# Kernel optimization log

Measured on AMD Instinct MI355X. Metric: run time of the kernel, lower is better.

## Reference

```python
import jax, jax.numpy as jnp
import numpy as np

B, S, D, H, DK = 2, 2048, 1024, 16, 64
NEG = -1000000000.0


def setup_inputs() -> dict:
    key = jax.random.key(0)
    ks = jax.random.split(key, 7)
    scale = 1.0 / np.sqrt(D)
    return {
        "pos_encode_toks": jax.random.normal(ks[0], (B, S, D), dtype=jnp.float32),
        "Wq": jax.random.uniform(ks[1], (D, D), minval=-scale, maxval=scale, dtype=jnp.float32),
        "bq": jax.random.uniform(ks[2], (D,), minval=-scale, maxval=scale, dtype=jnp.float32),
        "Wk": jax.random.uniform(ks[3], (D, D), minval=-scale, maxval=scale, dtype=jnp.float32),
        "bk": jax.random.uniform(ks[4], (D,), minval=-scale, maxval=scale, dtype=jnp.float32),
        "W0": jax.random.uniform(ks[5], (D, D), minval=-scale, maxval=scale, dtype=jnp.float32),
        "b0": jax.random.uniform(ks[6], (D,), minval=-scale, maxval=scale, dtype=jnp.float32),
    }


def reference(pos_encode_toks, Wq, bq, Wk, bk, W0, b0):
    x = pos_encode_toks
    b, s, d = x.shape
    # NOTE: the original module computes V with Wq (a bug in the source) -- replicated here.
    q = (x @ Wq + bq).reshape(b, s, H, DK).transpose(0, 2, 1, 3)  # [B,H,S,DK]
    k = (x @ Wk + bk).reshape(b, s, H, DK).transpose(0, 2, 1, 3)
    v = q  # V = Wq(x), same projection as Q
    scores = jnp.einsum("bhqd,bhkd->bhqk", q, k) / np.sqrt(DK)
    causal = jnp.tril(jnp.ones((s, s), dtype=bool))
    scores = jnp.where(causal, scores, NEG)
    att_pat = jax.nn.softmax(scores, axis=-1)
    att = jnp.einsum("bhqk,bhkd->bhqd", att_pat, v)
    att = att.transpose(0, 2, 1, 3).reshape(b, s, d)
    return att @ W0 + b0
```

## Files before the change

kernel.cpp:

```cpp
#include <hip/hip_runtime.h>
#include <hip/hip_bf16.h>
#include <cstdint>
#include <cstddef>


#define AS1 __attribute__((address_space(1)))
#define AS3 __attribute__((address_space(3)))

typedef unsigned short u16;
typedef __attribute__((ext_vector_type(8))) short bf16x8;
typedef __attribute__((ext_vector_type(4))) float f32x4;

__device__ __forceinline__ u16 f2bf(float f) {
  uint32_t u = __builtin_bit_cast(uint32_t, f);
  u += 0x7fffu + ((u >> 16) & 1u);
  return (u16)(u >> 16);
}

__device__ __forceinline__ void gload16(const void* g, void* l) {
  __builtin_amdgcn_global_load_lds((const AS1 uint32_t*)(uintptr_t)g,
                                   (AS3 uint32_t*)(uintptr_t)l, 16, 0, 0);
}

__global__ __launch_bounds__(256) void cvt_x_kernel(const float* __restrict__ x,
                                                    u16* __restrict__ xb) {
  const int stride = gridDim.x * blockDim.x;
  int i = blockIdx.x * blockDim.x + threadIdx.x;
  const float4* x4 = (const float4*)x;
  ushort4* o4 = (ushort4*)xb;
  for (; i < 1048576; i += stride) {
    float4 v = x4[i];
    ushort4 o;
    o.x = f2bf(v.x); o.y = f2bf(v.y); o.z = f2bf(v.z); o.w = f2bf(v.w);
    o4[i] = o;
  }
}

__global__ __launch_bounds__(256) void transpose_w_kernel(
    const float* __restrict__ Wq, const float* __restrict__ Wk,
    const float* __restrict__ W0, u16* __restrict__ wqT,
    u16* __restrict__ wkT, u16* __restrict__ w0T) {
  const float* src; u16* dst;
  if (blockIdx.z == 0)      { src = Wq; dst = wqT; }
  else if (blockIdx.z == 1) { src = Wk; dst = wkT; }
  else                      { src = W0; dst = w0T; }
  __shared__ u16 T[64][65];
  const int k0 = blockIdx.y * 64, n0 = blockIdx.x * 64;
  const int c = threadIdx.x & 63, r0 = threadIdx.x >> 6;
#pragma unroll
  for (int i = 0; i < 16; ++i) {
    int r = i * 4 + r0;
    T[r][c] = f2bf(src[(size_t)(k0 + r) * 1024 + n0 + c]);
  }
  __syncthreads();
#pragma unroll
  for (int i = 0; i < 16; ++i) {
    int r = i * 4 + r0;
    dst[(size_t)(n0 + r) * 1024 + k0 + c] = T[c][r];
  }
}

__global__ __launch_bounds__(256) void transpose_q_kernel(const u16* __restrict__ q,
                                                          u16* __restrict__ qT) {
  const int bh = blockIdx.y;
  const int s0 = blockIdx.x * 64;
  const u16* src = q + (size_t)bh * 2048 * 64;
  u16* dst = qT + (size_t)bh * 64 * 2048;
  __shared__ u16 T[64][65];
  const int c = threadIdx.x & 63, r0 = threadIdx.x >> 6;
#pragma unroll
  for (int i = 0; i < 16; ++i) {
    int r = i * 4 + r0;
    T[r][c] = src[(size_t)(s0 + r) * 64 + c];
  }
  __syncthreads();
#pragma unroll
  for (int i = 0; i < 16; ++i) {
    int r = i * 4 + r0;
    dst[(size_t)r * 2048 + s0 + c] = T[c][r];
  }
}

template <int EPI, int NTILES>
__global__ __launch_bounds__(512, 4) void gemm_kernel(
    const u16* __restrict__ A, const u16* __restrict__ BT,
    const float* __restrict__ bias0, const float* __restrict__ bias1,
    u16* __restrict__ Oq, u16* __restrict__ Ok, float* __restrict__ Of) {
  __shared__ __align__(16) u16 As[128][64];
  __shared__ __align__(16) u16 Bs[128][64];
  const int tid = threadIdx.x, wid = tid >> 6, lane = tid & 63;
  const int l15 = lane & 15, lg = lane >> 4;
  constexpr int NH = NTILES / 2;
  const int bid = blockIdx.x;
  const int c = bid & 7, l = bid >> 3;
  const int m0 = ((c >> 1) * 8 + l / NH) * 128;
  const int n0 = ((c & 1) * NH + l % NH) * 128;
  const int wrow = (wid >> 2) * 64, wcol = (wid & 3) * 32;
  const int srow = lane >> 3;
  const int gz = ((lane & 7) ^ srow) * 8;

  f32x4 acc[4][2] = {};

  for (int k0 = 0; k0 < 1024; k0 += 64) {
#pragma unroll
    for (int i = 0; i < 2; ++i) {
      int ch = wid * 2 + i;
      gload16(&A[(size_t)(m0 + ch * 8 + srow) * 1024 + k0 + gz], &As[ch * 8][0]);
      gload16(&BT[(size_t)(n0 + ch * 8 + srow) * 1024 + k0 + gz], &Bs[ch * 8][0]);
    }
    __syncthreads();
#pragma unroll
    for (int kf = 0; kf < 2; ++kf) {
      const int cg = ((kf * 4 + lg) ^ (lane & 7)) * 8;
      bf16x8 af[4], bfr[2];
#pragma unroll
      for (int m = 0; m < 4; ++m)
        af[m] = *(const bf16x8*)&As[wrow + m * 16 + l15][cg];
#pragma unroll
      for (int n = 0; n < 2; ++n)
        bfr[n] = *(const bf16x8*)&Bs[wcol + n * 16 + l15][cg];
#pragma unroll
      for (int m = 0; m < 4; ++m)
#pragma unroll
        for (int n = 0; n < 2; ++n)
          acc[m][n] = __builtin_amdgcn_mfma_f32_16x16x32_bf16(af[m], bfr[n], acc[m][n], 0, 0, 0);
    }
    __syncthreads();
  }

  float bv[2];
#pragma unroll
  for (int n = 0; n < 2; ++n) {
    const int gn = n0 + wcol + n * 16 + l15;
    if constexpr (EPI == 0)
      bv[n] = (gn < 1024) ? bias0[gn] : bias1[gn - 1024];
    else
      bv[n] = bias0[gn];
  }
#pragma unroll
  for (int m = 0; m < 4; ++m) {
#pragma unroll
    for (int r = 0; r < 4; ++r) {
      const int gm = m0 + wrow + m * 16 + lg * 4 + r;
#pragma unroll
      for (int n = 0; n < 2; ++n) {
        const int gn = n0 + wcol + n * 16 + l15;
        float v = acc[m][n][r] + bv[n];
        if constexpr (EPI == 2) {
          Of[(size_t)gm * 1024 + gn] = v;
        } else {
          u16* dst = (gn < 1024) ? Oq : Ok;
          const int gg = gn & 1023;
          const int b = gm >> 11, s = gm & 2047;
          const int h = gg >> 6, dk = gg & 63;
          dst[(((size_t)(b * 16 + h)) * 2048 + s) * 64 + dk] = f2bf(v);
        }
      }
    }
  }
}

__global__ __launch_bounds__(256, 4) void attn_kernel(const u16* __restrict__ Q,
                                                      const u16* __restrict__ K,
                                                      const u16* __restrict__ QT,
                                                      u16* __restrict__ ATT) {
  __shared__ __align__(16) u16 Ks[2][64][64];
  __shared__ __align__(16) u16 Vs[2][64][64];
  __shared__ __align__(16) u16 Ps[4][16][64];
  const int tid = threadIdx.x, wid = tid >> 6, lane = tid & 63;
  const int l15 = lane & 15, lg = lane >> 4;
  const int bid = blockIdx.x;
  const int bh = bid & 31;
  const int qt = 31 - (bid >> 5);
  const size_t base = (size_t)bh * 2048 * 64;
  const int bb = bh >> 4, hh = bh & 15;
  const int srow = lane >> 3;
  const int gz = ((lane & 7) ^ srow) * 8;
  const float SCALE2 = 0.18033688011112042f;

  const int q0 = qt * 64;
  const int wrow = q0 + wid * 16;

  bf16x8 qf[2];
#pragma unroll
  for (int kf = 0; kf < 2; ++kf)
    qf[kf] = *(const bf16x8*)&Q[base + (size_t)(wrow + l15) * 64 + kf * 32 + lg * 8];

  f32x4 o[4] = {};
  float mx[4], sm[4];
#pragma unroll
  for (int r = 0; r < 4; ++r) { mx[r] = -3e38f; sm[r] = 0.f; }

#pragma unroll
  for (int i = 0; i < 2; ++i) {
    int ch = wid * 2 + i;
    gload16(&K[base + (size_t)(ch * 8 + srow) * 64 + gz], &Ks[0][ch * 8][0]);
    gload16(&QT[base + (size_t)(ch * 8 + srow) * 2048 + gz], &Vs[0][ch * 8][0]);
  }
  __syncthreads();

  for (int t = 0; t <= qt; ++t) {
    const int cur = t & 1;
    if (t < qt) {
      const int kv1 = (t + 1) * 64;
#pragma unroll
      for (int i = 0; i < 2; ++i) {
        int ch = wid * 2 + i;
        gload16(&K[base + (size_t)(kv1 + ch * 8 + srow) * 64 + gz], &Ks[cur ^ 1][ch * 8][0]);
        gload16(&QT[base + (size_t)(ch * 8 + srow) * 2048 + kv1 + gz], &Vs[cur ^ 1][ch * 8][0]);
      }
    }

    f32x4 sc[4] = {};
#pragma unroll
    for (int kf = 0; kf < 2; ++kf) {
      const int cg = ((kf * 4 + lg) ^ (lane & 7)) * 8;
      bf16x8 kb[4];
#pragma unroll
      for (int n = 0; n < 4; ++n)
        kb[n] = *(const bf16x8*)&Ks[cur][n * 16 + l15][cg];
      __builtin_amdgcn_s_setprio(1);
#pragma unroll
      for (int n = 0; n < 4; ++n)
        sc[n] = __builtin_amdgcn_mfma_f32_16x16x32_bf16(qf[kf], kb[n], sc[n], 0, 0, 0);
      __builtin_amdgcn_s_setprio(0);
    }

    const bool maskt = (t == qt);
    float pr[4][4], rmax[4];
#pragma unroll
    for (int n = 0; n < 4; ++n)
#pragma unroll
      for (int r = 0; r < 4; ++r) {
        float v = sc[n][r] * SCALE2;
        if (maskt && (n * 16 + l15 > wid * 16 + lg * 4 + r)) v = -1e30f;
        pr[n][r] = v;
      }
#pragma unroll
    for (int r = 0; r < 4; ++r) {
      rmax[r] = fmaxf(fmaxf(pr[0][r], pr[1][r]), fmaxf(pr[2][r], pr[3][r]));
#pragma unroll
      for (int d = 1; d < 16; d <<= 1)
        rmax[r] = fmaxf(rmax[r], __shfl_xor(rmax[r], d));
    }

    bool grow = false;
#pragma unroll
    for (int r = 0; r < 4; ++r) grow |= (rmax[r] > mx[r] + 8.0f);
    if (__any(grow)) {
#pragma unroll
      for (int r = 0; r < 4; ++r) {
        const float mnew = fmaxf(mx[r], rmax[r]);
        const float alpha = exp2f(mx[r] - mnew);
        mx[r] = mnew;
        sm[r] *= alpha;
#pragma unroll
        for (int n = 0; n < 4; ++n) o[n][r] *= alpha;
      }
    }
#pragma unroll
    for (int r = 0; r < 4; ++r) {
      float rs = 0.f;
#pragma unroll
      for (int n = 0; n < 4; ++n) {
        const float p = exp2f(pr[n][r] - mx[r]);
        pr[n][r] = p;
        rs += p;
      }
      sm[r] += rs;
    }

#pragma unroll
    for (int r = 0; r < 4; ++r) {
      const int prow = lg * 4 + r;
      const int sw = (prow & 7) << 3;
      __hip_bfloat162 c01 = __float22bfloat162_rn(make_float2(pr[0][r], pr[1][r]));
      __hip_bfloat162 c23 = __float22bfloat162_rn(make_float2(pr[2][r], pr[3][r]));
      u16* pp = &Ps[wid][prow][0];
      pp[(l15)      ^ sw] = __builtin_bit_cast(u16, c01.x);
      pp[(16 + l15) ^ sw] = __builtin_bit_cast(u16, c01.y);
      pp[(32 + l15) ^ sw] = __builtin_bit_cast(u16, c23.x);
      pp[(48 + l15) ^ sw] = __builtin_bit_cast(u16, c23.y);
    }
    asm volatile("s_waitcnt lgkmcnt(0)" ::: "memory");

#pragma unroll
    for (int kf = 0; kf < 2; ++kf) {
      const int cg = ((kf * 4 + lg) ^ (lane & 7)) * 8;
      bf16x8 pa = *(const bf16x8*)&Ps[wid][l15][cg];
      bf16x8 vb[4];
#pragma unroll
      for (int n = 0; n < 4; ++n)
        vb[n] = *(const bf16x8*)&Vs[cur][n * 16 + l15][cg];
      __builtin_amdgcn_s_setprio(1);
#pragma unroll
      for (int n = 0; n < 4; ++n)
        o[n] = __builtin_amdgcn_mfma_f32_16x16x32_bf16(pa, vb[n], o[n], 0, 0, 0);
      __builtin_amdgcn_s_setprio(0);
    }
    __syncthreads();
  }

#pragma unroll
  for (int r = 0; r < 4; ++r)
#pragma unroll
    for (int d = 1; d < 16; d <<= 1) sm[r] += __shfl_xor(sm[r], d);

#pragma unroll
  for (int r = 0; r < 4; ++r) {
    const float inv = 1.0f / sm[r];
    const int s = wrow + lg * 4 + r;
    __hip_bfloat162 c01 = __float22bfloat162_rn(make_float2(o[0][r] * inv, o[1][r] * inv));
    __hip_bfloat162 c23 = __float22bfloat162_rn(make_float2(o[2][r] * inv, o[3][r] * inv));
    u16* dst = &ATT[((size_t)(bb * 2048 + s)) * 1024 + hh * 64 + l15];
    dst[0]  = __builtin_bit_cast(u16, c01.x);
    dst[16] = __builtin_bit_cast(u16, c01.y);
    dst[32] = __builtin_bit_cast(u16, c23.x);
    dst[48] = __builtin_bit_cast(u16, c23.y);
  }
}

extern "C" void kernel_launch(void* const* d_in, const int* in_sizes, int n_in,
                              void* d_out, int out_size, void* d_ws, size_t ws_size,
                              hipStream_t stream) {
  const float* x  = (const float*)d_in[0];
  const float* Wq = (const float*)d_in[1];
  const float* bq = (const float*)d_in[2];
  const float* Wk = (const float*)d_in[3];
  const float* bk = (const float*)d_in[4];
  const float* W0 = (const float*)d_in[5];
  const float* b0 = (const float*)d_in[6];
  float* out = (float*)d_out;

  char* ws = (char*)d_ws;
  u16* xb  = (u16*)(ws + 0);
  u16* wqT = (u16*)(ws + 8388608);
  u16* wkT = (u16*)(ws + 10485760);
  u16* w0T = (u16*)(ws + 12582912);
  u16* q   = (u16*)(ws + 14680064);
  u16* k   = (u16*)(ws + 23068672);
  u16* qT  = (u16*)(ws + 31457280);
  u16* att = (u16*)(ws + 39845888);

  cvt_x_kernel<<<dim3(1024), dim3(256), 0, stream>>>(x, xb);
  transpose_w_kernel<<<dim3(16, 16, 3), dim3(256), 0, stream>>>(Wq, Wk, W0, wqT, wkT, w0T);
  gemm_kernel<0, 16><<<dim3(512), dim3(512), 0, stream>>>(xb, wqT, bq, bk, q, k, nullptr);
  transpose_q_kernel<<<dim3(32, 32), dim3(256), 0, stream>>>(q, qT);
  attn_kernel<<<dim3(1024), dim3(256), 0, stream>>>(q, k, qT, att);
  gemm_kernel<2, 8><<<dim3(256), dim3(512), 0, stream>>>(att, w0T, b0, nullptr, nullptr, nullptr, out);
}
```

Measured before the change: 183.8 us.

## Fuse prep kernels, write Q transpose from GEMM, transpose attention score layout

Merges the x conversion and weight transpose into one launch, and drops the separate Q transpose kernel by having the QK projection GEMM epilogue also write Q transposed. The softmax scale is folded into K at projection time. The attention MFMAs are swapped to compute S^T so each lane owns one query row, which cuts the row reductions to two shuffles and allows packed P and output stores. The price is strided scalar stores for the transposed Q in the GEMM epilogue, plus rounding K to bf16 after scaling.

```diff
diff --git a/kernel.cpp b/kernel.cpp
--- a/kernel.cpp
+++ b/kernel.cpp
@@ -16,36 +16,42 @@
   u += 0x7fffu + ((u >> 16) & 1u);
   return (u16)(u >> 16);
 }
+__device__ __forceinline__ uint32_t pk2bf(float a, float b) {
+  return (uint32_t)f2bf(a) | ((uint32_t)f2bf(b) << 16);
+}
 
 __device__ __forceinline__ void gload16(const void* g, void* l) {
   __builtin_amdgcn_global_load_lds((const AS1 uint32_t*)(uintptr_t)g,
                                    (AS3 uint32_t*)(uintptr_t)l, 16, 0, 0);
 }
 
-__global__ __launch_bounds__(256) void cvt_x_kernel(const float* __restrict__ x,
-                                                    u16* __restrict__ xb) {
-  const int stride = gridDim.x * blockDim.x;
-  int i = blockIdx.x * blockDim.x + threadIdx.x;
-  const float4* x4 = (const float4*)x;
-  ushort4* o4 = (ushort4*)xb;
-  for (; i < 1048576; i += stride) {
-    float4 v = x4[i];
-    ushort4 o;
-    o.x = f2bf(v.x); o.y = f2bf(v.y); o.z = f2bf(v.z); o.w = f2bf(v.w);
-    o4[i] = o;
-  }
-}
-
-__global__ __launch_bounds__(256) void transpose_w_kernel(
+#define SCALE2 0.18033688011112042f
+
+__global__ __launch_bounds__(256) void prep_kernel(
+    const float* __restrict__ x, u16* __restrict__ xb,
     const float* __restrict__ Wq, const float* __restrict__ Wk,
     const float* __restrict__ W0, u16* __restrict__ wqT,
     u16* __restrict__ wkT, u16* __restrict__ w0T) {
+  __shared__ u16 T[64][65];
+  const int bid = blockIdx.x;
+  if (bid < 1024) {
+    const float4* x4 = (const float4*)x;
+    ushort4* o4 = (ushort4*)xb;
+    for (int i = bid * 256 + threadIdx.x; i < 1048576; i += 262144) {
+      float4 v = x4[i];
+      ushort4 o;
+      o.x = f2bf(v.x); o.y = f2bf(v.y); o.z = f2bf(v.z); o.w = f2bf(v.w);
+      o4[i] = o;
+    }
+    return;
+  }
+  const int t = bid - 1024;
+  const int z = t >> 8, y = (t >> 4) & 15, xt = t & 15;
   const float* src; u16* dst;
-  if (blockIdx.z == 0)      { src = Wq; dst = wqT; }
-  else if (blockIdx.z == 1) { src = Wk; dst = wkT; }
-  else                      { src = W0; dst = w0T; }
-  __shared__ u16 T[64][65];
-  const int k0 = blockIdx.y * 64, n0 = blockIdx.x * 64;
+  if (z == 0)      { src = Wq; dst = wqT; }
+  else if (z == 1) { src = Wk; dst = wkT; }
+  else             { src = W0; dst = w0T; }
+  const int k0 = y * 64, n0 = xt * 64;
   const int c = threadIdx.x & 63, r0 = threadIdx.x >> 6;
 #pragma unroll
   for (int i = 0; i < 16; ++i) {
@@ -57,27 +63,6 @@
   for (int i = 0; i < 16; ++i) {
     int r = i * 4 + r0;
     dst[(size_t)(n0 + r) * 1024 + k0 + c] = T[c][r];
-  }
-}
-
-__global__ __launch_bounds__(256) void transpose_q_kernel(const u16* __restrict__ q,
-                                                          u16* __restrict__ qT) {
-  const int bh = blockIdx.y;
-  const int s0 = blockIdx.x * 64;
-  const u16* src = q + (size_t)bh * 2048 * 64;
-  u16* dst = qT + (size_t)bh * 64 * 2048;
-  __shared__ u16 T[64][65];
-  const int c = threadIdx.x & 63, r0 = threadIdx.x >> 6;
-#pragma unroll
-  for (int i = 0; i < 16; ++i) {
-    int r = i * 4 + r0;
-    T[r][c] = src[(size_t)(s0 + r) * 64 + c];
-  }
-  __syncthreads();
-#pragma unroll
-  for (int i = 0; i < 16; ++i) {
-    int r = i * 4 + r0;
-    dst[(size_t)r * 2048 + s0 + c] = T[c][r];
   }
 }
 
@@ -85,7 +70,8 @@
 __global__ __launch_bounds__(512, 4) void gemm_kernel(
     const u16* __restrict__ A, const u16* __restrict__ BT,
     const float* __restrict__ bias0, const float* __restrict__ bias1,
-    u16* __restrict__ Oq, u16* __restrict__ Ok, float* __restrict__ Of) {
+    u16* __restrict__ Oq, u16* __restrict__ Ok, u16* __restrict__ OqT,
+    float* __restrict__ Of) {
   __shared__ __align__(16) u16 As[128][64];
   __shared__ __align__(16) u16 Bs[128][64];
   const int tid = threadIdx.x, wid = tid >> 6, lane = tid & 63;
@@ -128,12 +114,13 @@
     __syncthreads();
   }
 
+  const bool isq = (n0 < 1024);
   float bv[2];
 #pragma unroll
   for (int n = 0; n < 2; ++n) {
     const int gn = n0 + wcol + n * 16 + l15;
     if constexpr (EPI == 0)
-      bv[n] = (gn < 1024) ? bias0[gn] : bias1[gn - 1024];
+      bv[n] = isq ? bias0[gn] : bias1[gn - 1024];
     else
       bv[n] = bias0[gn];
   }
@@ -149,11 +136,17 @@
         if constexpr (EPI == 2) {
           Of[(size_t)gm * 1024 + gn] = v;
         } else {
-          u16* dst = (gn < 1024) ? Oq : Ok;
           const int gg = gn & 1023;
           const int b = gm >> 11, s = gm & 2047;
           const int h = gg >> 6, dk = gg & 63;
-          dst[(((size_t)(b * 16 + h)) * 2048 + s) * 64 + dk] = f2bf(v);
+          const size_t bh = (size_t)(b * 16 + h);
+          if (isq) {
+            const u16 qb = f2bf(v);
+            Oq[(bh * 2048 + s) * 64 + dk] = qb;
+            OqT[(bh * 64 + dk) * 2048 + s] = qb;
+          } else {
+            Ok[(bh * 2048 + s) * 64 + dk] = f2bf(v * SCALE2);
+          }
         }
       }
     }
@@ -176,7 +169,6 @@
   const int bb = bh >> 4, hh = bh & 15;
   const int srow = lane >> 3;
   const int gz = ((lane & 7) ^ srow) * 8;
-  const float SCALE2 = 0.18033688011112042f;
 
   const int q0 = qt * 64;
   const int wrow = q0 + wid * 16;
@@ -187,9 +179,7 @@
     qf[kf] = *(const bf16x8*)&Q[base + (size_t)(wrow + l15) * 64 + kf * 32 + lg * 8];
 
   f32x4 o[4] = {};
-  float mx[4], sm[4];
-#pragma unroll
-  for (int r = 0; r < 4; ++r) { mx[r] = -3e38f; sm[r] = 0.f; }
+  float mx = -3e38f, sm = 0.f;
 
 #pragma unroll
   for (int i = 0; i < 2; ++i) {
@@ -222,101 +212,83 @@
       __builtin_amdgcn_s_setprio(1);
 #pragma unroll
       for (int n = 0; n < 4; ++n)
-        sc[n] = __builtin_amdgcn_mfma_f32_16x16x32_bf16(qf[kf], kb[n], sc[n], 0, 0, 0);
+        sc[n] = __builtin_amdgcn_mfma_f32_16x16x32_bf16(kb[n], qf[kf], sc[n], 0, 0, 0);
       __builtin_amdgcn_s_setprio(0);
     }
 
-    const bool maskt = (t == qt);
-    float pr[4][4], rmax[4];
-#pragma unroll
-    for (int n = 0; n < 4; ++n)
-#pragma unroll
-      for (int r = 0; r < 4; ++r) {
-        float v = sc[n][r] * SCALE2;
-        if (maskt && (n * 16 + l15 > wid * 16 + lg * 4 + r)) v = -1e30f;
-        pr[n][r] = v;
-      }
-#pragma unroll
-    for (int r = 0; r < 4; ++r) {
-      rmax[r] = fmaxf(fmaxf(pr[0][r], pr[1][r]), fmaxf(pr[2][r], pr[3][r]));
-#pragma unroll
-      for (int d = 1; d < 16; d <<= 1)
-        rmax[r] = fmaxf(rmax[r], __shfl_xor(rmax[r], d));
-    }
-
-    bool grow = false;
-#pragma unroll
-    for (int r = 0; r < 4; ++r) grow |= (rmax[r] > mx[r] + 8.0f);
-    if (__any(grow)) {
-#pragma unroll
-      for (int r = 0; r < 4; ++r) {
-        const float mnew = fmaxf(mx[r], rmax[r]);
-        const float alpha = exp2f(mx[r] - mnew);
-        mx[r] = mnew;
-        sm[r] *= alpha;
-#pragma unroll
-        for (int n = 0; n < 4; ++n) o[n][r] *= alpha;
-      }
-    }
-#pragma unroll
-    for (int r = 0; r < 4; ++r) {
-      float rs = 0.f;
-#pragma unroll
-      for (int n = 0; n < 4; ++n) {
-        const float p = exp2f(pr[n][r] - mx[r]);
-        pr[n][r] = p;
-        rs += p;
-      }
-      sm[r] += rs;
-    }
-
-#pragma unroll
-    for (int r = 0; r < 4; ++r) {
-      const int prow = lg * 4 + r;
-      const int sw = (prow & 7) << 3;
-      __hip_bfloat162 c01 = __float22bfloat162_rn(make_float2(pr[0][r], pr[1][r]));
-      __hip_bfloat162 c23 = __float22bfloat162_rn(make_float2(pr[2][r], pr[3][r]));
-      u16* pp = &Ps[wid][prow][0];
-      pp[(l15)      ^ sw] = __builtin_bit_cast(u16, c01.x);
-      pp[(16 + l15) ^ sw] = __builtin_bit_cast(u16, c01.y);
-      pp[(32 + l15) ^ sw] = __builtin_bit_cast(u16, c23.x);
-      pp[(48 + l15) ^ sw] = __builtin_bit_cast(u16, c23.y);
+    if (t == qt) {
+      const int qq = wid * 16 + l15;
+#pragma unroll
+      for (int n = 0; n < 4; ++n)
+#pragma unroll
+        for (int r = 0; r < 4; ++r)
+          if (n * 16 + lg * 4 + r > qq) sc[n][r] = -1e30f;
+    }
+
+    float ma = fmaxf(fmaxf(sc[0][0], sc[0][1]), fmaxf(sc[0][2], sc[0][3]));
+    float mb = fmaxf(fmaxf(sc[1][0], sc[1][1]), fmaxf(sc[1][2], sc[1][3]));
+    float mc = fmaxf(fmaxf(sc[2][0], sc[2][1]), fmaxf(sc[2][2], sc[2][3]));
+    float md = fmaxf(fmaxf(sc[3][0], sc[3][1]), fmaxf(sc[3][2], sc[3][3]));
+    float rmax = fmaxf(fmaxf(ma, mb), fmaxf(mc, md));
+    rmax = fmaxf(rmax, __shfl_xor(rmax, 16));
+    rmax = fmaxf(rmax, __shfl_xor(rmax, 32));
+
+    if (__any(rmax > mx + 8.0f)) {
+      const float mnew = fmaxf(mx, rmax);
+      const float alpha = exp2f(mx - mnew);
+      mx = mnew;
+      sm *= alpha;
+#pragma unroll
+      for (int m = 0; m < 4; ++m) o[m] *= alpha;
+    }
+
+    float psum = 0.f;
+    uint32_t w[4][2];
+#pragma unroll
+    for (int n = 0; n < 4; ++n) {
+      const float p0 = exp2f(sc[n][0] - mx), p1 = exp2f(sc[n][1] - mx);
+      const float p2 = exp2f(sc[n][2] - mx), p3 = exp2f(sc[n][3] - mx);
+      psum += (p0 + p1) + (p2 + p3);
+      w[n][0] = pk2bf(p0, p1);
+      w[n][1] = pk2bf(p2, p3);
+    }
+    sm += psum;
+
+#pragma unroll
+    for (int n = 0; n < 4; ++n) {
+      const int col = (((2 * n + (lg >> 1)) ^ (l15 & 7)) << 3) + ((lg & 1) << 2);
+      uint2 wv; wv.x = w[n][0]; wv.y = w[n][1];
+      *(uint2*)&Ps[wid][l15][col] = wv;
     }
     asm volatile("s_waitcnt lgkmcnt(0)" ::: "memory");
 
 #pragma unroll
     for (int kf = 0; kf < 2; ++kf) {
       const int cg = ((kf * 4 + lg) ^ (lane & 7)) * 8;
-      bf16x8 pa = *(const bf16x8*)&Ps[wid][l15][cg];
+      bf16x8 pb = *(const bf16x8*)&Ps[wid][l15][cg];
       bf16x8 vb[4];
 #pragma unroll
-      for (int n = 0; n < 4; ++n)
-        vb[n] = *(const bf16x8*)&Vs[cur][n * 16 + l15][cg];
+      for (int m = 0; m < 4; ++m)
+        vb[m] = *(const bf16x8*)&Vs[cur][m * 16 + l15][cg];
       __builtin_amdgcn_s_setprio(1);
 #pragma unroll
-      for (int n = 0; n < 4; ++n)
-        o[n] = __builtin_amdgcn_mfma_f32_16x16x32_bf16(pa, vb[n], o[n], 0, 0, 0);
+      for (int m = 0; m < 4; ++m)
+        o[m] = __builtin_amdgcn_mfma_f32_16x16x32_bf16(vb[m], pb, o[m], 0, 0, 0);
       __builtin_amdgcn_s_setprio(0);
     }
     __syncthreads();
   }
 
-#pragma unroll
-  for (int r = 0; r < 4; ++r)
-#pragma unroll
-    for (int d = 1; d < 16; d <<= 1) sm[r] += __shfl_xor(sm[r], d);
-
-#pragma unroll
-  for (int r = 0; r < 4; ++r) {
-    const float inv = 1.0f / sm[r];
-    const int s = wrow + lg * 4 + r;
-    __hip_bfloat162 c01 = __float22bfloat162_rn(make_float2(o[0][r] * inv, o[1][r] * inv));
-    __hip_bfloat162 c23 = __float22bfloat162_rn(make_float2(o[2][r] * inv, o[3][r] * inv));
-    u16* dst = &ATT[((size_t)(bb * 2048 + s)) * 1024 + hh * 64 + l15];
-    dst[0]  = __builtin_bit_cast(u16, c01.x);
-    dst[16] = __builtin_bit_cast(u16, c01.y);
-    dst[32] = __builtin_bit_cast(u16, c23.x);
-    dst[48] = __builtin_bit_cast(u16, c23.y);
+  sm += __shfl_xor(sm, 16);
+  sm += __shfl_xor(sm, 32);
+  const float inv = 1.0f / sm;
+  const int s = wrow + l15;
+#pragma unroll
+  for (int m = 0; m < 4; ++m) {
+    uint2 wv;
+    wv.x = pk2bf(o[m][0] * inv, o[m][1] * inv);
+    wv.y = pk2bf(o[m][2] * inv, o[m][3] * inv);
+    *(uint2*)&ATT[((size_t)(bb * 2048 + s)) * 1024 + hh * 64 + m * 16 + lg * 4] = wv;
   }
 }
 
@@ -342,10 +314,8 @@
   u16* qT  = (u16*)(ws + 31457280);
   u16* att = (u16*)(ws + 39845888);
 
-  cvt_x_kernel<<<dim3(1024), dim3(256), 0, stream>>>(x, xb);
-  transpose_w_kernel<<<dim3(16, 16, 3), dim3(256), 0, stream>>>(Wq, Wk, W0, wqT, wkT, w0T);
-  gemm_kernel<0, 16><<<dim3(512), dim3(512), 0, stream>>>(xb, wqT, bq, bk, q, k, nullptr);
-  transpose_q_kernel<<<dim3(32, 32), dim3(256), 0, stream>>>(q, qT);
+  prep_kernel<<<dim3(1792), dim3(256), 0, stream>>>(x, xb, Wq, Wk, W0, wqT, wkT, w0T);
+  gemm_kernel<0, 16><<<dim3(512), dim3(512), 0, stream>>>(xb, wqT, bq, bk, q, k, qT, nullptr);
   attn_kernel<<<dim3(1024), dim3(256), 0, stream>>>(q, k, qT, att);
-  gemm_kernel<2, 8><<<dim3(256), dim3(512), 0, stream>>>(att, w0T, b0, nullptr, nullptr, nullptr, out);
-}
+  gemm_kernel<2, 8><<<dim3(256), dim3(512), 0, stream>>>(att, w0T, b0, nullptr, nullptr, nullptr, nullptr, out);
+}
```

Measured after the change: 181.4 us. About the same (-1.3%).
